# Kernel optimization log

Measured on AMD Instinct MI355X. Metric: run time of the kernel, lower is better.

## Reference

```python
import jax, jax.numpy as jnp
import numpy as np

B, T, D, H, C = 64, 1024, 128, 512, 2


def setup_inputs() -> dict:
    key = jax.random.key(0)
    ks = jax.random.split(key, 6)
    x = jax.random.normal(ks[0], (B, T, D), dtype=jnp.float32)
    labels = jax.random.randint(ks[1], (B, T), 0, C, dtype=jnp.int32)
    # Keras LSTMCell params: kernel [D,4H], recurrent_kernel [H,4H], bias [4H]
    Wx = jax.random.normal(ks[2], (D, 4 * H), dtype=jnp.float32) * (1.0 / np.sqrt(D))
    Wh = jax.random.normal(ks[3], (H, 4 * H), dtype=jnp.float32) * (1.0 / np.sqrt(H))
    b = jnp.zeros((4 * H,), dtype=jnp.float32).at[H:2 * H].set(1.0)  # unit forget bias
    Wo = jax.random.normal(ks[4], (H, C), dtype=jnp.float32) * (1.0 / np.sqrt(H))
    bo = jnp.zeros((C,), dtype=jnp.float32)
    return {"x": x, "labels": labels, "Wx": Wx, "Wh": Wh, "b": b, "Wo": Wo, "bo": bo}


def _lstm_logits(x, Wx, Wh, b, Wo, bo):
    # Precompute input contribution for all steps: [B,T,4H]
    xz = jnp.einsum('btd,dk->btk', x, Wx) + b

    def step(carry, z_t):
        h, c = carry
        z = z_t + h @ Wh                     # [B,4H]
        i, f, g, o = jnp.split(z, 4, axis=-1)  # keras gate order: i,f,c,o
        i = jax.nn.sigmoid(i)
        f = jax.nn.sigmoid(f)
        g = jnp.tanh(g)
        o = jax.nn.sigmoid(o)
        c = f * c + i * g
        h = o * jnp.tanh(c)
        return (h, c), h

    h0 = jnp.zeros((x.shape[0], Wh.shape[0]), dtype=x.dtype)
    (_, _), hs = jax.lax.scan(step, (h0, h0), jnp.swapaxes(xz, 0, 1))
    hs = jnp.swapaxes(hs, 0, 1)              # [B,T,H]
    return jnp.einsum('bth,hc->btc', hs, Wo) + bo  # [B,T,C]


def reference(x, labels, Wx, Wh, b, Wo, bo):
    logits = _lstm_logits(x, Wx, Wh, b, Wo, bo)
    logp = jax.nn.log_softmax(logits, axis=-1)
    prediction = jnp.exp(logp)               # softmax probs
    nll = -jnp.take_along_axis(logp, labels[..., None].astype(jnp.int32), axis=-1)[..., 0]
    cost = jnp.mean(nll)
    return prediction, cost
```

## Files before the change

kernel.cpp:

```cpp
#include <hip/hip_runtime.h>
#include <stdint.h>

#define TLEN 1024
#define BATCH 64
#define DIMX 128
#define HID 512

typedef __attribute__((ext_vector_type(8))) short short8;
typedef __attribute__((ext_vector_type(4))) float f32x4;
typedef __attribute__((ext_vector_type(4))) unsigned u32x4;

#define OFF_WT   0u
#define OFF_XBF  2621440u
#define OFF_HB   19398656u
#define OFF_ACC  19660800u
#define OFF_PART 19660864u
#define ZERO_LEN 262208u

__device__ __forceinline__ unsigned short f2bf(float f) {
  unsigned u = __float_as_uint(f);
  u += 0x7fffu + ((u >> 16) & 1u);
  return (unsigned short)(u >> 16);
}
__device__ __forceinline__ float sigm(float x) { return 1.0f / (1.0f + __expf(-x)); }
__device__ __forceinline__ float tanh_fast(float x) {
  float a = fabsf(x);
  float e = __expf(2.0f * a);
  float t = 1.0f - 2.0f / (e + 1.0f);
  return copysignf(t, x);
}

__device__ __forceinline__ bool tags_bad(const u32x4& r0, const u32x4& r1,
                                         const u32x4& r2, const u32x4& r3,
                                         unsigned tg) {
  unsigned d = (r0[0] ^ tg) | (r0[1] ^ tg) | (r0[2] ^ tg) | (r0[3] ^ tg);
  d |= (r1[0] ^ tg) | (r1[1] ^ tg) | (r1[2] ^ tg) | (r1[3] ^ tg);
  d |= (r2[0] ^ tg) | (r2[1] ^ tg) | (r2[2] ^ tg) | (r2[3] ^ tg);
  d |= (r3[0] ^ tg) | (r3[1] ^ tg) | (r3[2] ^ tg) | (r3[3] ^ tg);
  return (d & 0xFFFFu) != 0u;
}

__global__ void k_convx(const float4* __restrict__ x4, ushort4* __restrict__ o4) {
  int i = blockIdx.x * 256 + threadIdx.x;
  float4 v = x4[i];
  ushort4 o;
  o.x = f2bf(v.x); o.y = f2bf(v.y); o.z = f2bf(v.z); o.w = f2bf(v.w);
  o4[i] = o;
}

__global__ void k_tw(const float* __restrict__ Wx, const float* __restrict__ Wh,
                     unsigned short* __restrict__ Wt) {
  __shared__ float tile[32][65];
  int bk = blockIdx.x;
  int k0 = (bk / 64) * 64;
  int c0 = (bk % 64) * 32;
  int tid = threadIdx.x;
  const float* src = (k0 < 128) ? (Wx + (size_t)k0 * 2048)
                                : (Wh + (size_t)(k0 - 128) * 2048);
#pragma unroll
  for (int p = 0; p < 8; ++p) {
    int i = p * 256 + tid;
    int kk = i >> 5, cc = i & 31;
    tile[cc][kk] = src[(size_t)kk * 2048 + (c0 + cc)];
  }
  __syncthreads();
  int cc = tid >> 3, ch = tid & 7;
  unsigned short tmp[8];
#pragma unroll
  for (int j = 0; j < 8; ++j) tmp[j] = f2bf(tile[cc][ch * 8 + j]);
  uint4 o;
  o.x = (unsigned)tmp[0] | ((unsigned)tmp[1] << 16);
  o.y = (unsigned)tmp[2] | ((unsigned)tmp[3] << 16);
  o.z = (unsigned)tmp[4] | ((unsigned)tmp[5] << 16);
  o.w = (unsigned)tmp[6] | ((unsigned)tmp[7] << 16);
  *(uint4*)(Wt + (size_t)(c0 + cc) * 640 + k0 + ch * 8) = o;
}

__global__ __launch_bounds__(512, 1) void k_lstm(
    const unsigned short* __restrict__ xbf,
    const unsigned short* __restrict__ Wt,
    const float* __restrict__ bias,
    const float* __restrict__ Wo,
    unsigned* __restrict__ hb,
    float* __restrict__ part)
{
  __shared__ float red[2][4][4][8][32];
  __shared__ short8 xch[2][4][2][2][64];
  __shared__ unsigned xflag[2][4][2];

  const int tid  = threadIdx.x;
  const int w    = tid >> 6;
  const int kw   = w & 3;
  const int cg   = w >> 2;
  const int lane = tid & 63;
  const int q    = lane >> 4;
  const int m    = lane & 15;
  const int grp  = blockIdx.x & 7;
  const int hj   = blockIdx.x >> 3;
  const int g0   = grp * 8;

  if (tid < 16) xflag[tid >> 3][(tid >> 1) & 3][tid & 1] = 0;

  short8 Bf[5][4];
#pragma unroll
  for (int cc = 0; cc < 5; ++cc) {
#pragma unroll
    for (int j = 0; j < 4; ++j) {
      int gate = cg * 2 + (j >> 1);
      int col = gate * HID + hj * 32 + (j & 1) * 16 + m;
      int k = (cc == 0) ? (kw * 32 + q * 8)
                        : (128 + kw * 128 + (cc - 1) * 32 + q * 8);
      Bf[cc][j] = *(const short8*)(Wt + (size_t)col * 640 + k);
    }
  }

  const int col  = lane & 31;
  const int hcol = hj * 32 + col;
  float c_state = 0.0f;
  const float b_i = bias[0 * HID + hcol];
  const float b_f = bias[1 * HID + hcol];
  const float b_g = bias[2 * HID + hcol];
  const float b_o = bias[3 * HID + hcol];
  const float2 wo = ((const float2*)Wo)[hcol];

  const int arow = (m < 8) ? m : 7;
  const int ab = g0 + arow;
  const size_t poff = (size_t)ab * HID + kw * 128 + cg * 64 + q * 8;

  __syncthreads();

#pragma unroll 1
  for (int t = 0; t < TLEN; ++t) {
    const unsigned* hin = hb + (size_t)(t & 1) * (BATCH * HID);
    const int buf = t & 1;

    short8 a0 = *(const short8*)(xbf + ((size_t)ab * TLEN + t) * DIMX +
                                 kw * 32 + q * 8);
    f32x4 z0 = {0,0,0,0}, z1 = {0,0,0,0}, z2 = {0,0,0,0}, z3 = {0,0,0,0};
    z0 = __builtin_amdgcn_mfma_f32_16x16x32_bf16(a0, Bf[0][0], z0, 0, 0, 0);
    z1 = __builtin_amdgcn_mfma_f32_16x16x32_bf16(a0, Bf[0][1], z1, 0, 0, 0);
    z2 = __builtin_amdgcn_mfma_f32_16x16x32_bf16(a0, Bf[0][2], z2, 0, 0, 0);
    z3 = __builtin_amdgcn_mfma_f32_16x16x32_bf16(a0, Bf[0][3], z3, 0, 0, 0);

    const unsigned* pb = hin + poff;
    u32x4 r0, r1, r2, r3;
    {
      const unsigned tg = (unsigned)t & 0xFFFFu;
      int guard = 0;
      for (;;) {
        asm volatile(
            "global_load_dwordx4 %0, %4, off sc0 sc1\n\t"
            "global_load_dwordx4 %1, %4, off offset:16 sc0 sc1\n\t"
            "global_load_dwordx4 %2, %4, off offset:128 sc0 sc1\n\t"
            "global_load_dwordx4 %3, %4, off offset:144 sc0 sc1\n\t"
            "s_waitcnt vmcnt(0)"
            : "=v"(r0), "=v"(r1), "=v"(r2), "=v"(r3)
            : "v"(pb)
            : "memory");
        bool bad = tags_bad(r0, r1, r2, r3, tg);
        if (__ballot(bad) == 0ull || ++guard > (1 << 20)) break;
      }
    }

    short8 f0, f1;
    {
      union { short8 s; unsigned u[4]; } pk;
      pk.u[0] = (r0[0] >> 16) | (r0[1] & 0xFFFF0000u);
      pk.u[1] = (r0[2] >> 16) | (r0[3] & 0xFFFF0000u);
      pk.u[2] = (r1[0] >> 16) | (r1[1] & 0xFFFF0000u);
      pk.u[3] = (r1[2] >> 16) | (r1[3] & 0xFFFF0000u);
      f0 = pk.s;
      pk.u[0] = (r2[0] >> 16) | (r2[1] & 0xFFFF0000u);
      pk.u[1] = (r2[2] >> 16) | (r2[3] & 0xFFFF0000u);
      pk.u[2] = (r3[0] >> 16) | (r3[1] & 0xFFFF0000u);
      pk.u[3] = (r3[2] >> 16) | (r3[3] & 0xFFFF0000u);
      f1 = pk.s;
    }

    xch[buf][kw][cg][0][lane] = f0;
    xch[buf][kw][cg][1][lane] = f1;
    __hip_atomic_store(&xflag[buf][kw][cg], (unsigned)(t + 1),
                       __ATOMIC_RELEASE, __HIP_MEMORY_SCOPE_WORKGROUP);
    {
      int guard = 0;
      while (__hip_atomic_load(&xflag[buf][kw][cg ^ 1], __ATOMIC_ACQUIRE,
                               __HIP_MEMORY_SCOPE_WORKGROUP) < (unsigned)(t + 1)) {
        if (++guard > (1 << 22)) break;
      }
    }
    short8 s0 = xch[buf][kw][cg ^ 1][0][lane];
    short8 s1 = xch[buf][kw][cg ^ 1][1][lane];

    short8 a1 = cg ? s0 : f0;
    short8 a2 = cg ? s1 : f1;
    short8 a3 = cg ? f0 : s0;
    short8 a4 = cg ? f1 : s1;

    z0 = __builtin_amdgcn_mfma_f32_16x16x32_bf16(a1, Bf[1][0], z0, 0, 0, 0);
    z1 = __builtin_amdgcn_mfma_f32_16x16x32_bf16(a1, Bf[1][1], z1, 0, 0, 0);
    z2 = __builtin_amdgcn_mfma_f32_16x16x32_bf16(a1, Bf[1][2], z2, 0, 0, 0);
    z3 = __builtin_amdgcn_mfma_f32_16x16x32_bf16(a1, Bf[1][3], z3, 0, 0, 0);
    z0 = __builtin_amdgcn_mfma_f32_16x16x32_bf16(a2, Bf[2][0], z0, 0, 0, 0);
    z1 = __builtin_amdgcn_mfma_f32_16x16x32_bf16(a2, Bf[2][1], z1, 0, 0, 0);
    z2 = __builtin_amdgcn_mfma_f32_16x16x32_bf16(a2, Bf[2][2], z2, 0, 0, 0);
    z3 = __builtin_amdgcn_mfma_f32_16x16x32_bf16(a2, Bf[2][3], z3, 0, 0, 0);
    z0 = __builtin_amdgcn_mfma_f32_16x16x32_bf16(a3, Bf[3][0], z0, 0, 0, 0);
    z1 = __builtin_amdgcn_mfma_f32_16x16x32_bf16(a3, Bf[3][1], z1, 0, 0, 0);
    z2 = __builtin_amdgcn_mfma_f32_16x16x32_bf16(a3, Bf[3][2], z2, 0, 0, 0);
    z3 = __builtin_amdgcn_mfma_f32_16x16x32_bf16(a3, Bf[3][3], z3, 0, 0, 0);
    z0 = __builtin_amdgcn_mfma_f32_16x16x32_bf16(a4, Bf[4][0], z0, 0, 0, 0);
    z1 = __builtin_amdgcn_mfma_f32_16x16x32_bf16(a4, Bf[4][1], z1, 0, 0, 0);
    z2 = __builtin_amdgcn_mfma_f32_16x16x32_bf16(a4, Bf[4][2], z2, 0, 0, 0);
    z3 = __builtin_amdgcn_mfma_f32_16x16x32_bf16(a4, Bf[4][3], z3, 0, 0, 0);

    if (q < 2) {
#pragma unroll
      for (int r = 0; r < 4; ++r) {
        int rw = q * 4 + r;
        red[buf][kw][cg * 2 + 0][rw][0 * 16 + m] = z0[r];
        red[buf][kw][cg * 2 + 0][rw][1 * 16 + m] = z1[r];
        red[buf][kw][cg * 2 + 1][rw][0 * 16 + m] = z2[r];
        red[buf][kw][cg * 2 + 1][rw][1 * 16 + m] = z3[r];
      }
    }
    __syncthreads();

    if (lane < 32) {
      float zi = b_i + red[buf][0][0][w][col] + red[buf][1][0][w][col]
                     + red[buf][2][0][w][col] + red[buf][3][0][w][col];
      float zf = b_f + red[buf][0][1][w][col] + red[buf][1][1][w][col]
                     + red[buf][2][1][w][col] + red[buf][3][1][w][col];
      float zg = b_g + red[buf][0][2][w][col] + red[buf][1][2][w][col]
                     + red[buf][2][2][w][col] + red[buf][3][2][w][col];
      float zo = b_o + red[buf][0][3][w][col] + red[buf][1][3][w][col]
                     + red[buf][2][3][w][col] + red[buf][3][3][w][col];
      float ig = sigm(zi), fg = sigm(zf), gg = tanh_fast(zg), og = sigm(zo);
      c_state = fg * c_state + ig * gg;
      float hval = og * tanh_fast(c_state);

      unsigned hword = ((unsigned)f2bf(hval) << 16) | (unsigned)((t + 1) & 0xFFFF);
      unsigned* dst = hb + (size_t)((t + 1) & 1) * (BATCH * HID) +
                      (size_t)(g0 + w) * HID + hcol;
      asm volatile("global_store_dword %0, %1, off sc0 sc1"
                   :: "v"(dst), "v"(hword) : "memory");

      float p0 = hval * wo.x, p1 = hval * wo.y;
      p0 += __shfl_xor(p0, 16); p1 += __shfl_xor(p1, 16);
      p0 += __shfl_xor(p0, 8);  p1 += __shfl_xor(p1, 8);
      p0 += __shfl_xor(p0, 4);  p1 += __shfl_xor(p1, 4);
      p0 += __shfl_xor(p0, 2);  p1 += __shfl_xor(p1, 2);
      p0 += __shfl_xor(p0, 1);  p1 += __shfl_xor(p1, 1);
      if (lane == 0) {
        float2 pv; pv.x = p0; pv.y = p1;
        *(float2*)(part + (((size_t)hj * BATCH + (g0 + w)) * TLEN + t) * 2) = pv;
      }
    }
  }
}

__global__ void k_out2(float* __restrict__ out, const float* __restrict__ bo,
                       const int* __restrict__ labels,
                       const float2* __restrict__ part,
                       float* __restrict__ acc) {
  __shared__ float sred[4];
  int i = blockIdx.x * 256 + threadIdx.x;
  float l0 = bo[0], l1 = bo[1];
#pragma unroll
  for (int hj = 0; hj < 16; ++hj) {
    float2 p = part[(size_t)hj * (BATCH * TLEN) + i];
    l0 += p.x; l1 += p.y;
  }
  float mx = fmaxf(l0, l1);
  float e0 = __expf(l0 - mx), e1 = __expf(l1 - mx);
  float s = e0 + e1, inv = 1.0f / s;
  out[(size_t)i * 2 + 0] = e0 * inv;
  out[(size_t)i * 2 + 1] = e1 * inv;
  int lab = labels[i];
  float nll = __logf(s) - ((lab ? l1 : l0) - mx);
#pragma unroll
  for (int off = 32; off >= 1; off >>= 1) nll += __shfl_xor(nll, off);
  if ((threadIdx.x & 63) == 0) sred[threadIdx.x >> 6] = nll;
  __syncthreads();
  if (threadIdx.x == 0)
    atomicAdd(acc, sred[0] + sred[1] + sred[2] + sred[3]);
}

__global__ void k_fin(const float* __restrict__ acc, float* __restrict__ out) {
  out[BATCH * TLEN * 2] = acc[0] * (1.0f / (float)(BATCH * TLEN));
}

extern "C" void kernel_launch(void* const* d_in, const int* in_sizes, int n_in,
                              void* d_out, int out_size, void* d_ws, size_t ws_size,
                              hipStream_t stream) {
  const float* x      = (const float*)d_in[0];
  const int*   labels = (const int*)d_in[1];
  const float* Wx     = (const float*)d_in[2];
  const float* Wh     = (const float*)d_in[3];
  const float* b      = (const float*)d_in[4];
  const float* Wo     = (const float*)d_in[5];
  const float* bo     = (const float*)d_in[6];
  float* out = (float*)d_out;
  char* ws = (char*)d_ws;

  unsigned short* Wt  = (unsigned short*)(ws + OFF_WT);
  unsigned short* xbf = (unsigned short*)(ws + OFF_XBF);
  unsigned*       hb  = (unsigned*)(ws + OFF_HB);
  float*          acc = (float*)(ws + OFF_ACC);
  float*          part = (float*)(ws + OFF_PART);

  hipMemsetAsync(ws + OFF_HB, 0, ZERO_LEN, stream);
  k_convx<<<8192, 256, 0, stream>>>((const float4*)x, (ushort4*)xbf);
  k_tw<<<640, 256, 0, stream>>>(Wx, Wh, Wt);
  k_lstm<<<128, 512, 0, stream>>>(xbf, Wt, b, Wo, hb, part);
  k_out2<<<256, 256, 0, stream>>>(out, bo, labels, (const float2*)part, acc);
  k_fin<<<1, 1, 0, stream>>>(acc, out);
}
```

Measured before the change: 2.900 ms.

## Replace cross-wave LDS flag exchange of h fragments with intra-wave shuffles

Each wave previously loaded half of its h-state rows from global memory, published them to shared memory with a release flag, and spun on the partner wave's flag to get the other half. Now the lanes of each 16-lane group load rows from both halves, selected by lane index, and the A fragments are assembled with __shfl permutations inside the wave. This removes the LDS exchange and the cross-wave spin-wait from the per-timestep critical path. The cost is 16 extra shuffles per step, and the first MFMA batch now issues after the h load instead of overlapping with it.

```diff
diff --git a/kernel.cpp b/kernel.cpp
--- a/kernel.cpp
+++ b/kernel.cpp
@@ -85,8 +85,6 @@
     float* __restrict__ part)
 {
   __shared__ float red[2][4][4][8][32];
-  __shared__ short8 xch[2][4][2][2][64];
-  __shared__ unsigned xflag[2][4][2];
 
   const int tid  = threadIdx.x;
   const int w    = tid >> 6;
@@ -99,8 +97,6 @@
   const int hj   = blockIdx.x >> 3;
   const int g0   = grp * 8;
 
-  if (tid < 16) xflag[tid >> 3][(tid >> 1) & 3][tid & 1] = 0;
-
   short8 Bf[5][4];
 #pragma unroll
   for (int cc = 0; cc < 5; ++cc) {
@@ -125,7 +121,14 @@
 
   const int arow = (m < 8) ? m : 7;
   const int ab = g0 + arow;
-  const size_t poff = (size_t)ab * HID + kw * 128 + cg * 64 + q * 8;
+
+  const int rowm = m & 7;
+  const int hf   = cg ^ (m >> 3);
+  const size_t poffF = (size_t)(g0 + rowm) * HID + kw * 128 + hf * 64 + q * 8;
+
+  const int sbase = lane & ~15;
+  const int src0 = sbase + rowm + cg * 8;
+  const int src1 = sbase + rowm + (cg ^ 1) * 8;
 
   __syncthreads();
 
@@ -136,13 +139,8 @@
 
     short8 a0 = *(const short8*)(xbf + ((size_t)ab * TLEN + t) * DIMX +
                                  kw * 32 + q * 8);
-    f32x4 z0 = {0,0,0,0}, z1 = {0,0,0,0}, z2 = {0,0,0,0}, z3 = {0,0,0,0};
-    z0 = __builtin_amdgcn_mfma_f32_16x16x32_bf16(a0, Bf[0][0], z0, 0, 0, 0);
-    z1 = __builtin_amdgcn_mfma_f32_16x16x32_bf16(a0, Bf[0][1], z1, 0, 0, 0);
-    z2 = __builtin_amdgcn_mfma_f32_16x16x32_bf16(a0, Bf[0][2], z2, 0, 0, 0);
-    z3 = __builtin_amdgcn_mfma_f32_16x16x32_bf16(a0, Bf[0][3], z3, 0, 0, 0);
-
-    const unsigned* pb = hin + poff;
+
+    const unsigned* pb = hin + poffF;
     u32x4 r0, r1, r2, r3;
     {
       const unsigned tg = (unsigned)t & 0xFFFFu;
@@ -162,40 +160,32 @@
       }
     }
 
-    short8 f0, f1;
-    {
-      union { short8 s; unsigned u[4]; } pk;
-      pk.u[0] = (r0[0] >> 16) | (r0[1] & 0xFFFF0000u);
-      pk.u[1] = (r0[2] >> 16) | (r0[3] & 0xFFFF0000u);
-      pk.u[2] = (r1[0] >> 16) | (r1[1] & 0xFFFF0000u);
-      pk.u[3] = (r1[2] >> 16) | (r1[3] & 0xFFFF0000u);
-      f0 = pk.s;
-      pk.u[0] = (r2[0] >> 16) | (r2[1] & 0xFFFF0000u);
-      pk.u[1] = (r2[2] >> 16) | (r2[3] & 0xFFFF0000u);
-      pk.u[2] = (r3[0] >> 16) | (r3[1] & 0xFFFF0000u);
-      pk.u[3] = (r3[2] >> 16) | (r3[3] & 0xFFFF0000u);
-      f1 = pk.s;
-    }
-
-    xch[buf][kw][cg][0][lane] = f0;
-    xch[buf][kw][cg][1][lane] = f1;
-    __hip_atomic_store(&xflag[buf][kw][cg], (unsigned)(t + 1),
-                       __ATOMIC_RELEASE, __HIP_MEMORY_SCOPE_WORKGROUP);
-    {
-      int guard = 0;
-      while (__hip_atomic_load(&xflag[buf][kw][cg ^ 1], __ATOMIC_ACQUIRE,
-                               __HIP_MEMORY_SCOPE_WORKGROUP) < (unsigned)(t + 1)) {
-        if (++guard > (1 << 22)) break;
-      }
-    }
-    short8 s0 = xch[buf][kw][cg ^ 1][0][lane];
-    short8 s1 = xch[buf][kw][cg ^ 1][1][lane];
-
-    short8 a1 = cg ? s0 : f0;
-    short8 a2 = cg ? s1 : f1;
-    short8 a3 = cg ? f0 : s0;
-    short8 a4 = cg ? f1 : s1;
-
+    union U4 { short8 s; unsigned u[4]; };
+    U4 F0, F1;
+    F0.u[0] = (r0[0] >> 16) | (r0[1] & 0xFFFF0000u);
+    F0.u[1] = (r0[2] >> 16) | (r0[3] & 0xFFFF0000u);
+    F0.u[2] = (r1[0] >> 16) | (r1[1] & 0xFFFF0000u);
+    F0.u[3] = (r1[2] >> 16) | (r1[3] & 0xFFFF0000u);
+    F1.u[0] = (r2[0] >> 16) | (r2[1] & 0xFFFF0000u);
+    F1.u[1] = (r2[2] >> 16) | (r2[3] & 0xFFFF0000u);
+    F1.u[2] = (r3[0] >> 16) | (r3[1] & 0xFFFF0000u);
+    F1.u[3] = (r3[2] >> 16) | (r3[3] & 0xFFFF0000u);
+
+    U4 A1, A2, A3, A4;
+#pragma unroll
+    for (int j = 0; j < 4; ++j) {
+      A1.u[j] = __shfl(F0.u[j], src0);
+      A2.u[j] = __shfl(F1.u[j], src0);
+      A3.u[j] = __shfl(F0.u[j], src1);
+      A4.u[j] = __shfl(F1.u[j], src1);
+    }
+    short8 a1 = A1.s, a2 = A2.s, a3 = A3.s, a4 = A4.s;
+
+    f32x4 z0 = {0,0,0,0}, z1 = {0,0,0,0}, z2 = {0,0,0,0}, z3 = {0,0,0,0};
+    z0 = __builtin_amdgcn_mfma_f32_16x16x32_bf16(a0, Bf[0][0], z0, 0, 0, 0);
+    z1 = __builtin_amdgcn_mfma_f32_16x16x32_bf16(a0, Bf[0][1], z1, 0, 0, 0);
+    z2 = __builtin_amdgcn_mfma_f32_16x16x32_bf16(a0, Bf[0][2], z2, 0, 0, 0);
+    z3 = __builtin_amdgcn_mfma_f32_16x16x32_bf16(a0, Bf[0][3], z3, 0, 0, 0);
     z0 = __builtin_amdgcn_mfma_f32_16x16x32_bf16(a1, Bf[1][0], z0, 0, 0, 0);
     z1 = __builtin_amdgcn_mfma_f32_16x16x32_bf16(a1, Bf[1][1], z1, 0, 0, 0);
     z2 = __builtin_amdgcn_mfma_f32_16x16x32_bf16(a1, Bf[1][2], z2, 0, 0, 0);
```

Result: slower. 3.644 ms (+25.7%).

## Split recurrent K across all 8 waves, drop intra-block h exchange

Applied to the files above, without the earlier changes.

Each of the 8 waves now owns a 64-wide K slice of the recurrent matmul across all four gates, instead of waves pairing up over gate groups. This removes the per-step LDS exchange of loaded h fragments between paired waves and its spin-wait flag. In exchange each wave issues 16–24 MFMAs per step rather than 20, and the gate reduction reads 8 partials instead of 4, doubling the LDS reduction buffer. The input projection is split across waves 0–3 only, which makes per-wave work uneven.

```diff
diff --git a/kernel.cpp b/kernel.cpp
--- a/kernel.cpp
+++ b/kernel.cpp
@@ -84,14 +84,10 @@
     unsigned* __restrict__ hb,
     float* __restrict__ part)
 {
-  __shared__ float red[2][4][4][8][32];
-  __shared__ short8 xch[2][4][2][2][64];
-  __shared__ unsigned xflag[2][4][2];
+  __shared__ float red[2][8][4][8][32];
 
   const int tid  = threadIdx.x;
   const int w    = tid >> 6;
-  const int kw   = w & 3;
-  const int cg   = w >> 2;
   const int lane = tid & 63;
   const int q    = lane >> 4;
   const int m    = lane & 15;
@@ -99,19 +95,17 @@
   const int hj   = blockIdx.x >> 3;
   const int g0   = grp * 8;
 
-  if (tid < 16) xflag[tid >> 3][(tid >> 1) & 3][tid & 1] = 0;
-
-  short8 Bf[5][4];
-#pragma unroll
-  for (int cc = 0; cc < 5; ++cc) {
-#pragma unroll
-    for (int j = 0; j < 4; ++j) {
-      int gate = cg * 2 + (j >> 1);
-      int col = gate * HID + hj * 32 + (j & 1) * 16 + m;
-      int k = (cc == 0) ? (kw * 32 + q * 8)
-                        : (128 + kw * 128 + (cc - 1) * 32 + q * 8);
-      Bf[cc][j] = *(const short8*)(Wt + (size_t)col * 640 + k);
-    }
+  short8 Bh[8][2];
+  short8 Bx[8];
+#pragma unroll
+  for (int f = 0; f < 8; ++f) {
+    int gate = f >> 1;
+    int colg = gate * HID + hj * 32 + (f & 1) * 16 + m;
+    const unsigned short* wc = Wt + (size_t)colg * 640;
+#pragma unroll
+    for (int c = 0; c < 2; ++c)
+      Bh[f][c] = *(const short8*)(wc + 128 + w * 64 + c * 32 + q * 8);
+    if (w < 4) Bx[f] = *(const short8*)(wc + w * 32 + q * 8);
   }
 
   const int col  = lane & 31;
@@ -125,7 +119,7 @@
 
   const int arow = (m < 8) ? m : 7;
   const int ab = g0 + arow;
-  const size_t poff = (size_t)ab * HID + kw * 128 + cg * 64 + q * 8;
+  const size_t poff = (size_t)ab * HID + w * 64 + q * 8;
 
   __syncthreads();
 
@@ -134,13 +128,10 @@
     const unsigned* hin = hb + (size_t)(t & 1) * (BATCH * HID);
     const int buf = t & 1;
 
-    short8 a0 = *(const short8*)(xbf + ((size_t)ab * TLEN + t) * DIMX +
-                                 kw * 32 + q * 8);
-    f32x4 z0 = {0,0,0,0}, z1 = {0,0,0,0}, z2 = {0,0,0,0}, z3 = {0,0,0,0};
-    z0 = __builtin_amdgcn_mfma_f32_16x16x32_bf16(a0, Bf[0][0], z0, 0, 0, 0);
-    z1 = __builtin_amdgcn_mfma_f32_16x16x32_bf16(a0, Bf[0][1], z1, 0, 0, 0);
-    z2 = __builtin_amdgcn_mfma_f32_16x16x32_bf16(a0, Bf[0][2], z2, 0, 0, 0);
-    z3 = __builtin_amdgcn_mfma_f32_16x16x32_bf16(a0, Bf[0][3], z3, 0, 0, 0);
+    short8 a0;
+    if (w < 4)
+      a0 = *(const short8*)(xbf + ((size_t)ab * TLEN + t) * DIMX +
+                            w * 32 + q * 8);
 
     const unsigned* pb = hin + poff;
     u32x4 r0, r1, r2, r3;
@@ -162,78 +153,55 @@
       }
     }
 
-    short8 f0, f1;
+    short8 af0, af1;
     {
       union { short8 s; unsigned u[4]; } pk;
       pk.u[0] = (r0[0] >> 16) | (r0[1] & 0xFFFF0000u);
       pk.u[1] = (r0[2] >> 16) | (r0[3] & 0xFFFF0000u);
       pk.u[2] = (r1[0] >> 16) | (r1[1] & 0xFFFF0000u);
       pk.u[3] = (r1[2] >> 16) | (r1[3] & 0xFFFF0000u);
-      f0 = pk.s;
+      af0 = pk.s;
       pk.u[0] = (r2[0] >> 16) | (r2[1] & 0xFFFF0000u);
       pk.u[1] = (r2[2] >> 16) | (r2[3] & 0xFFFF0000u);
       pk.u[2] = (r3[0] >> 16) | (r3[1] & 0xFFFF0000u);
       pk.u[3] = (r3[2] >> 16) | (r3[3] & 0xFFFF0000u);
-      f1 = pk.s;
-    }
-
-    xch[buf][kw][cg][0][lane] = f0;
-    xch[buf][kw][cg][1][lane] = f1;
-    __hip_atomic_store(&xflag[buf][kw][cg], (unsigned)(t + 1),
-                       __ATOMIC_RELEASE, __HIP_MEMORY_SCOPE_WORKGROUP);
-    {
-      int guard = 0;
-      while (__hip_atomic_load(&xflag[buf][kw][cg ^ 1], __ATOMIC_ACQUIRE,
-                               __HIP_MEMORY_SCOPE_WORKGROUP) < (unsigned)(t + 1)) {
-        if (++guard > (1 << 22)) break;
-      }
-    }
-    short8 s0 = xch[buf][kw][cg ^ 1][0][lane];
-    short8 s1 = xch[buf][kw][cg ^ 1][1][lane];
-
-    short8 a1 = cg ? s0 : f0;
-    short8 a2 = cg ? s1 : f1;
-    short8 a3 = cg ? f0 : s0;
-    short8 a4 = cg ? f1 : s1;
-
-    z0 = __builtin_amdgcn_mfma_f32_16x16x32_bf16(a1, Bf[1][0], z0, 0, 0, 0);
-    z1 = __builtin_amdgcn_mfma_f32_16x16x32_bf16(a1, Bf[1][1], z1, 0, 0, 0);
-    z2 = __builtin_amdgcn_mfma_f32_16x16x32_bf16(a1, Bf[1][2], z2, 0, 0, 0);
-    z3 = __builtin_amdgcn_mfma_f32_16x16x32_bf16(a1, Bf[1][3], z3, 0, 0, 0);
-    z0 = __builtin_amdgcn_mfma_f32_16x16x32_bf16(a2, Bf[2][0], z0, 0, 0, 0);
-    z1 = __builtin_amdgcn_mfma_f32_16x16x32_bf16(a2, Bf[2][1], z1, 0, 0, 0);
-    z2 = __builtin_amdgcn_mfma_f32_16x16x32_bf16(a2, Bf[2][2], z2, 0, 0, 0);
-    z3 = __builtin_amdgcn_mfma_f32_16x16x32_bf16(a2, Bf[2][3], z3, 0, 0, 0);
-    z0 = __builtin_amdgcn_mfma_f32_16x16x32_bf16(a3, Bf[3][0], z0, 0, 0, 0);
-    z1 = __builtin_amdgcn_mfma_f32_16x16x32_bf16(a3, Bf[3][1], z1, 0, 0, 0);
-    z2 = __builtin_amdgcn_mfma_f32_16x16x32_bf16(a3, Bf[3][2], z2, 0, 0, 0);
-    z3 = __builtin_amdgcn_mfma_f32_16x16x32_bf16(a3, Bf[3][3], z3, 0, 0, 0);
-    z0 = __builtin_amdgcn_mfma_f32_16x16x32_bf16(a4, Bf[4][0], z0, 0, 0, 0);
-    z1 = __builtin_amdgcn_mfma_f32_16x16x32_bf16(a4, Bf[4][1], z1, 0, 0, 0);
-    z2 = __builtin_amdgcn_mfma_f32_16x16x32_bf16(a4, Bf[4][2], z2, 0, 0, 0);
-    z3 = __builtin_amdgcn_mfma_f32_16x16x32_bf16(a4, Bf[4][3], z3, 0, 0, 0);
+      af1 = pk.s;
+    }
+
+    f32x4 z[8];
+#pragma unroll
+    for (int f = 0; f < 8; ++f) z[f] = (f32x4){0.f, 0.f, 0.f, 0.f};
+    if (w < 4) {
+#pragma unroll
+      for (int f = 0; f < 8; ++f)
+        z[f] = __builtin_amdgcn_mfma_f32_16x16x32_bf16(a0, Bx[f], z[f], 0, 0, 0);
+    }
+#pragma unroll
+    for (int f = 0; f < 8; ++f)
+      z[f] = __builtin_amdgcn_mfma_f32_16x16x32_bf16(af0, Bh[f][0], z[f], 0, 0, 0);
+#pragma unroll
+    for (int f = 0; f < 8; ++f)
+      z[f] = __builtin_amdgcn_mfma_f32_16x16x32_bf16(af1, Bh[f][1], z[f], 0, 0, 0);
 
     if (q < 2) {
 #pragma unroll
-      for (int r = 0; r < 4; ++r) {
-        int rw = q * 4 + r;
-        red[buf][kw][cg * 2 + 0][rw][0 * 16 + m] = z0[r];
-        red[buf][kw][cg * 2 + 0][rw][1 * 16 + m] = z1[r];
-        red[buf][kw][cg * 2 + 1][rw][0 * 16 + m] = z2[r];
-        red[buf][kw][cg * 2 + 1][rw][1 * 16 + m] = z3[r];
+      for (int f = 0; f < 8; ++f) {
+#pragma unroll
+        for (int r = 0; r < 4; ++r)
+          red[buf][w][f >> 1][q * 4 + r][(f & 1) * 16 + m] = z[f][r];
       }
     }
     __syncthreads();
 
     if (lane < 32) {
-      float zi = b_i + red[buf][0][0][w][col] + red[buf][1][0][w][col]
-                     + red[buf][2][0][w][col] + red[buf][3][0][w][col];
-      float zf = b_f + red[buf][0][1][w][col] + red[buf][1][1][w][col]
-                     + red[buf][2][1][w][col] + red[buf][3][1][w][col];
-      float zg = b_g + red[buf][0][2][w][col] + red[buf][1][2][w][col]
-                     + red[buf][2][2][w][col] + red[buf][3][2][w][col];
-      float zo = b_o + red[buf][0][3][w][col] + red[buf][1][3][w][col]
-                     + red[buf][2][3][w][col] + red[buf][3][3][w][col];
+      float zi = b_i, zf = b_f, zg = b_g, zo = b_o;
+#pragma unroll
+      for (int jj = 0; jj < 8; ++jj) {
+        zi += red[buf][jj][0][w][col];
+        zf += red[buf][jj][1][w][col];
+        zg += red[buf][jj][2][w][col];
+        zo += red[buf][jj][3][w][col];
+      }
       float ig = sigm(zi), fg = sigm(zf), gg = tanh_fast(zg), og = sigm(zo);
       c_state = fg * c_state + ig * gg;
       float hval = og * tanh_fast(c_state);
```

New measurement: 2.748 ms. -5.2%, faster.
